# Optimization experiments

Hardware: AMD Instinct MI355X
Metric: run time of the kernel (lower is better)

Reference implementation:

```python
import jax, jax.numpy as jnp
import numpy as np

N = 4096          # vocab / support size (Nini == Nfin)
NBB = 64          # number of topics (columns of b)
NUM_ITER_MAX = 30
STOP_THR = 1e-9


def setup_inputs() -> dict:
    key = jax.random.key(0)
    k1, k2, k3, k4 = jax.random.split(key, 4)
    a = jax.random.uniform(k1, (N, 1), dtype=jnp.float32)
    a = a / jnp.sum(a)                       # source distribution
    b = jax.random.uniform(k2, (N, NBB), dtype=jnp.float32)
    b = b / jnp.sum(b, axis=0, keepdims=True)  # each column a distribution
    lbd = jax.random.uniform(k3, (NBB, 1), dtype=jnp.float32)
    lbd = lbd / jnp.sum(lbd)                 # barycenter weights sum to 1
    M = jax.random.uniform(k4, (N, N), dtype=jnp.float32)  # cost matrix >= 0
    reg = jnp.float32(0.1)
    return {"a": a, "M": M, "b": b, "lbd": lbd, "reg": reg}


def reference(a, M, b, lbd, reg):
    C = jnp.exp(-M / reg)                    # expjit
    lbdT = lbd.T                             # (1, nbb)
    u0 = jnp.ones_like(b)                    # (N, nbb)
    v0 = jnp.ones_like(b)                    # (N, nbb)
    yhat0 = jnp.zeros_like(a)                # (N, 1)

    def cond(state):
        cpt, err, broke, u, v, yhat = state
        return (err > STOP_THR) & (cpt < NUM_ITER_MAX) & (~broke)

    def body(state):
        cpt, err, broke, u, v, yhat = state
        Cu = C @ u                                        # (N, nbb)
        v_new = C.T @ (b / Cu)                            # (N, nbb)
        yhat_new = jnp.prod(v_new ** lbdT, axis=1, keepdims=True)  # (N, 1)
        u_new = yhat_new / v_new                          # (N, nbb)
        bad = (jnp.any(Cu == 0)
               | ~jnp.all(jnp.isfinite(u_new))
               | ~jnp.all(jnp.isfinite(v_new))
               | ~jnp.all(jnp.isfinite(yhat_new)))
        # convergence check every 10 iterations (torch: cpt % 10 == 0)
        lhs = jnp.sum((u_new - u) ** 2) / jnp.sum(u_new ** 2)
        rhs = jnp.sum((v_new - v) ** 2) / jnp.sum(v_new ** 2)
        err_new = jnp.where((cpt % 10 == 0) & ~bad, lhs + rhs, err)
        # on numerical error: revert to previous iterates and break
        u2 = jnp.where(bad, u, u_new)
        v2 = jnp.where(bad, v, v_new)
        yhat2 = jnp.where(bad, yhat, yhat_new)
        cpt2 = cpt + jnp.where(bad, 0, 1)
        return (cpt2, err_new, bad, u2, v2, yhat2)

    state0 = (jnp.int32(0), jnp.float32(1.0), jnp.bool_(False), u0, v0, yhat0)
    *_, yhat = jax.lax.while_loop(cond, body, state0)
    # torch.norm(yhat - a) ** 2 == squared Frobenius norm
    return jnp.sum((yhat - a) ** 2)
```

## Files before the change

### kernel.cpp

```cpp
#include <hip/hip_runtime.h>


typedef __attribute__((ext_vector_type(8))) short bf16x8;
typedef __attribute__((ext_vector_type(4))) float f32x4;

constexpr int NV    = 4096;
constexpr int NBB_  = 64;
constexpr int ITERS = 30;

__device__ __forceinline__ bool finitef(float x) {
  return __builtin_fabsf(x) <= 3.402823466e38f;
}

__device__ __forceinline__ unsigned short f2bf(float x) {
  unsigned int u = __builtin_bit_cast(unsigned int, x);
  return (unsigned short)((u + 0x7fffu + ((u >> 16) & 1u)) >> 16);
}

__global__ void k_setup(float* __restrict__ u, float* __restrict__ v,
                        unsigned short* __restrict__ uT, float* __restrict__ yh,
                        float* __restrict__ S) {
  const int gid = blockIdx.x * 256 + threadIdx.x;
  for (int i = gid; i < NV * NBB_; i += 16384) {
    u[i] = 1.0f; v[i] = 1.0f; uT[i] = 0x3F80;
  }
  for (int i = gid; i < NV; i += 16384) yh[i] = 0.0f;
  if (gid == 0) {
    int* Si = (int*)S;
    S[0]  = 1.0f;
    Si[1] = 0;
    Si[2] = 0;
    Si[3] = 1; Si[4] = 0;
    Si[5] = 0; Si[6] = 0;
    Si[7] = 0; Si[8] = 0;
    for (int q = 16; q < 16 + ITERS; ++q) Si[q] = 0;
  }
}

__global__ void k_cgen(const float* __restrict__ M, const float* __restrict__ regp,
                       unsigned short* __restrict__ Cb,
                       unsigned short* __restrict__ CTb) {
  __shared__ float tile[64][65];
  const int jb = (blockIdx.x & 63) * 64;
  const int ib = (blockIdx.x >> 6) * 64;
  const float ninv = -1.0f / regp[0];
  const int t = threadIdx.x;
#pragma unroll
  for (int s = 0; s < 4; ++s) {
    const int l = s * 256 + t;
    const int r = l >> 4, c4 = l & 15;
    const float4 m4 = *(const float4*)&M[(size_t)(ib + r) * NV + jb + c4 * 4];
    float4 e4;
    e4.x = __expf(m4.x * ninv);
    e4.y = __expf(m4.y * ninv);
    e4.z = __expf(m4.z * ninv);
    e4.w = __expf(m4.w * ninv);
    ushort4 o;
    o.x = f2bf(e4.x); o.y = f2bf(e4.y); o.z = f2bf(e4.z); o.w = f2bf(e4.w);
    *(ushort4*)&Cb[(size_t)(ib + r) * NV + jb + c4 * 4] = o;
    *(float4*)&tile[r][c4 * 4] = e4;
  }
  __syncthreads();
#pragma unroll
  for (int s = 0; s < 4; ++s) {
    const int l = s * 256 + t;
    const int r = l >> 4, c4 = l & 15;
    ushort4 o;
    o.x = f2bf(tile[c4 * 4 + 0][r]);
    o.y = f2bf(tile[c4 * 4 + 1][r]);
    o.z = f2bf(tile[c4 * 4 + 2][r]);
    o.w = f2bf(tile[c4 * 4 + 3][r]);
    *(ushort4*)&CTb[(size_t)(jb + r) * NV + ib + c4 * 4] = o;
  }
}

#define GEMM_CORE(Abase, Bbase, red4)                                          \
  {                                                                            \
    const unsigned short* Ap = (Abase) + (size_t)(R + lr) * NV + w * 512 + lg * 8; \
    const unsigned short* Bp = (Bbase) + (size_t)lr * NV + w * 512 + lg * 8;   \
    f32x4 acc[4] = {};                                                         \
    bf16x8 abuf[3];                                                            \
    bf16x8 bbuf[3][4];                                                         \
    _Pragma("unroll")                                                          \
    for (int p = 0; p < 3; ++p) {                                              \
      abuf[p] = *(const bf16x8*)(Ap + 32 * p);                                 \
      _Pragma("unroll")                                                        \
      for (int ct = 0; ct < 4; ++ct)                                           \
        bbuf[p][ct] = *(const bf16x8*)(Bp + (size_t)ct * 16 * NV + 32 * p);    \
    }                                                                          \
    _Pragma("unroll")                                                          \
    for (int i = 0; i < 16; ++i) {                                             \
      const int sl = i % 3;                                                    \
      _Pragma("unroll")                                                        \
      for (int ct = 0; ct < 4; ++ct)                                           \
        acc[ct] = __builtin_amdgcn_mfma_f32_16x16x32_bf16(abuf[sl],            \
                                                          bbuf[sl][ct],        \
                                                          acc[ct], 0, 0, 0);   \
      if (i + 3 < 16) {                                                        \
        abuf[sl] = *(const bf16x8*)(Ap + 32 * (i + 3));                        \
        _Pragma("unroll")                                                      \
        for (int ct = 0; ct < 4; ++ct)                                         \
          bbuf[sl][ct] =                                                       \
              *(const bf16x8*)(Bp + (size_t)ct * 16 * NV + 32 * (i + 3));      \
      }                                                                        \
    }                                                                          \
    _Pragma("unroll")                                                          \
    for (int ct = 0; ct < 4; ++ct) red4[w][ct][lane] = acc[ct];                \
  }

__global__ __launch_bounds__(512, 2) void k_fwd1(
    const unsigned short* __restrict__ Cb, const unsigned short* __restrict__ uT,
    const float* __restrict__ b, unsigned short* __restrict__ rT,
    int* __restrict__ badflag, const int* __restrict__ act) {
  if (*act == 0) return;
  __shared__ f32x4 red4[8][4][64];
  const int R = blockIdx.x * 16;
  const int t = threadIdx.x, w = t >> 6, lane = t & 63;
  const int lr = lane & 15, lg = lane >> 4;
  GEMM_CORE(Cb, uT, red4)
  __syncthreads();
  if (w < 4) {
    const int ct = w;
    f32x4 cu = red4[0][ct][lane];
#pragma unroll
    for (int j = 1; j < 8; ++j) cu += red4[j][ct][lane];
    bool bad = false;
    float rq[4];
#pragma unroll
    for (int q = 0; q < 4; ++q) {
      const float cuq = cu[q];
      const float bq  = b[(R + lg * 4 + q) * NBB_ + ct * 16 + lr];
      bad |= (cuq == 0.0f);
      rq[q] = bq / cuq;
    }
    ushort4 rr;
    rr.x = f2bf(rq[0]); rr.y = f2bf(rq[1]); rr.z = f2bf(rq[2]); rr.w = f2bf(rq[3]);
    *(ushort4*)&rT[(size_t)(ct * 16 + lr) * NV + R + lg * 4] = rr;
    if (bad) atomicOr(badflag, 1);
  }
}

__global__ __launch_bounds__(512, 2) void k_fwd2(
    const unsigned short* __restrict__ CTb, const unsigned short* __restrict__ rT,
    const float* __restrict__ lbd, float* __restrict__ u, float* __restrict__ v,
    unsigned short* __restrict__ uT, float* __restrict__ yh,
    float* __restrict__ yhn, float* __restrict__ Spart, float* __restrict__ S,
    int it) {
  int* Si = (int*)S;
  const int slot = it & 1;
  if (Si[3 + slot] == 0) {
    if (blockIdx.x == 0 && threadIdx.x == 0) Si[3 + (slot ^ 1)] = 0;
    return;
  }
  __shared__ f32x4 red4[8][4][64];
  __shared__ float yred[4][16];
  __shared__ float yhl[16];
  __shared__ float wred[4][4];
  __shared__ float cred[8][4];
  __shared__ int   flags[2];
  const int R = blockIdx.x * 16;
  const int t = threadIdx.x, w = t >> 6, lane = t & 63;
  const int lr = lane & 15, lg = lane >> 4;
  GEMM_CORE(CTb, rT, red4)
  __syncthreads();
  f32x4 vv = {0.f, 0.f, 0.f, 0.f};
  if (w < 4) {
    vv = red4[0][w][lane];
#pragma unroll
    for (int j = 1; j < 8; ++j) vv += red4[j][w][lane];
    const float lb = lbd[w * 16 + lr];
    float p[4];
#pragma unroll
    for (int q = 0; q < 4; ++q) p[q] = lb * __logf(vv[q]);
#pragma unroll
    for (int o = 1; o < 16; o <<= 1) {
#pragma unroll
      for (int q = 0; q < 4; ++q) p[q] += __shfl_xor(p[q], o);
    }
    if (lr == 0) {
#pragma unroll
      for (int q = 0; q < 4; ++q) yred[w][lg * 4 + q] = p[q];
    }
  }
  __syncthreads();
  if (t < 16) {
    const float s   = yred[0][t] + yred[1][t] + yred[2][t] + yred[3][t];
    const float yhv = __expf(s);
    yhl[t] = yhv;
    yhn[R + t] = yhv;
    if (!finitef(yhv)) atomicOr(&Si[7 + slot], 1);
  }
  __syncthreads();
  if (w < 4) {
    float s0 = 0.f, s1 = 0.f, s2 = 0.f, s3 = 0.f;
    bool bad = false;
    float un4[4];
#pragma unroll
    for (int q = 0; q < 4; ++q) {
      const int   row = lg * 4 + q;
      const float yhv = yhl[row];
      const float un  = yhv / vv[q];
      un4[q] = un;
      const int idx = (R + row) * NBB_ + w * 16 + lr;
      const float uo = u[idx], vo = v[idx];
      u[idx] = un;
      v[idx] = vv[q];
      const float du = un - uo, dv = vv[q] - vo;
      s0 += du * du; s1 += un * un; s2 += dv * dv; s3 += vv[q] * vv[q];
      bad |= !(finitef(un) && finitef(vv[q]));
    }
    ushort4 uu;
    uu.x = f2bf(un4[0]); uu.y = f2bf(un4[1]); uu.z = f2bf(un4[2]); uu.w = f2bf(un4[3]);
    *(ushort4*)&uT[(size_t)(w * 16 + lr) * NV + R + lg * 4] = uu;
    if (bad) atomicOr(&Si[7 + slot], 1);
#pragma unroll
    for (int o = 1; o < 64; o <<= 1) {
      s0 += __shfl_xor(s0, o); s1 += __shfl_xor(s1, o);
      s2 += __shfl_xor(s2, o); s3 += __shfl_xor(s3, o);
    }
    if (lane == 0) {
      wred[w][0] = s0; wred[w][1] = s1; wred[w][2] = s2; wred[w][3] = s3;
    }
  }
  __syncthreads();
  if (t == 0) {
#pragma unroll
    for (int c = 0; c < 4; ++c)
      Spart[blockIdx.x * 4 + c] =
          wred[0][c] + wred[1][c] + wred[2][c] + wred[3][c];
    __threadfence();
    flags[0] = (atomicAdd(&Si[16 + it], 1) == (int)gridDim.x - 1);
  }
  __syncthreads();
  if (!flags[0]) return;
  __threadfence();
  {
    const int c   = t & 3;
    const int idx = t >> 2;
    float s = Spart[idx * 4 + c] + Spart[(idx + 128) * 4 + c];
#pragma unroll
    for (int o = 4; o < 64; o <<= 1) s += __shfl_xor(s, o);
    if (lane < 4) cred[w][lane] = s;
  }
  __syncthreads();
  if (t == 0) {
    float q0 = 0.f, q1 = 0.f, q2 = 0.f, q3 = 0.f;
#pragma unroll
    for (int i = 0; i < 8; ++i) {
      q0 += cred[i][0]; q1 += cred[i][1]; q2 += cred[i][2]; q3 += cred[i][3];
    }
    const bool bad = (Si[5 + slot] | Si[7 + slot]) != 0;
    int com = 0;
    if (!bad) {
      const int cpt = Si[1];
      if (cpt % 10 == 0) S[0] = q0 / q1 + q2 / q3;
      Si[1] = cpt + 1;
      com = 1;
    } else {
      Si[2] = 1;
    }
    const int ns = slot ^ 1;
    Si[3 + ns] = (S[0] > 1e-9f && Si[1] < ITERS && Si[2] == 0) ? 1 : 0;
    Si[5 + ns] = 0;
    Si[7 + ns] = 0;
    flags[1] = com;
  }
  __syncthreads();
  if (flags[1])
    for (int i = t; i < NV; i += 512) yh[i] = yhn[i];
}

__global__ void k_final(const float* __restrict__ yhat, const float* __restrict__ a,
                        float* __restrict__ out) {
  __shared__ float red[4];
  const int t = threadIdx.x;
  float s = 0.0f;
  for (int i = t; i < NV; i += 256) {
    const float d = yhat[i] - a[i];
    s = fmaf(d, d, s);
  }
#pragma unroll
  for (int o = 32; o > 0; o >>= 1) s += __shfl_xor(s, o);
  if ((t & 63) == 0) red[t >> 6] = s;
  __syncthreads();
  if (t == 0) out[0] = red[0] + red[1] + red[2] + red[3];
}

extern "C" void kernel_launch(void* const* d_in, const int* in_sizes, int n_in,
                              void* d_out, int out_size, void* d_ws, size_t ws_size,
                              hipStream_t stream) {
  const float* a   = (const float*)d_in[0];
  const float* M   = (const float*)d_in[1];
  const float* b   = (const float*)d_in[2];
  const float* lbd = (const float*)d_in[3];
  const float* reg = (const float*)d_in[4];
  float* out = (float*)d_out;

  char* wsb = (char*)d_ws;
  size_t off = 0;
  auto alloc = [&](size_t bytes) -> void* {
    void* p = wsb + off;
    off += (bytes + 255) & ~(size_t)255;
    return p;
  };
  unsigned short* Cbf   = (unsigned short*)alloc(2 * (size_t)NV * NV);
  unsigned short* CTbf  = (unsigned short*)alloc(2 * (size_t)NV * NV);
  unsigned short* uT    = (unsigned short*)alloc(2 * (size_t)NV * NBB_);
  unsigned short* rT    = (unsigned short*)alloc(2 * (size_t)NV * NBB_);
  float*          u     = (float*)alloc(sizeof(float) * (size_t)NV * NBB_);
  float*          v     = (float*)alloc(sizeof(float) * (size_t)NV * NBB_);
  float*          yh    = (float*)alloc(sizeof(float) * NV);
  float*          yhn   = (float*)alloc(sizeof(float) * NV);
  float*          S     = (float*)alloc(sizeof(float) * 64);
  float*          Spart = (float*)alloc(sizeof(float) * 256 * 4);
  int* Si = (int*)S;

  k_setup<<<dim3(64), dim3(256), 0, stream>>>(u, v, uT, yh, S);
  k_cgen<<<dim3(4096), dim3(256), 0, stream>>>(M, reg, Cbf, CTbf);

  for (int it = 0; it < ITERS; ++it) {
    const int slot = it & 1;
    const int* act = (const int*)(Si + 3 + slot);
    k_fwd1<<<dim3(256), dim3(512), 0, stream>>>(Cbf, uT, b, rT, Si + 5 + slot, act);
    k_fwd2<<<dim3(256), dim3(512), 0, stream>>>(CTbf, rT, lbd, u, v, uT, yh,
                                                yhn, Spart, S, it);
  }

  k_final<<<dim3(1), dim3(256), 0, stream>>>(yh, a, out);
}
```

Measured before the change: 1.237 ms.

## Fuse iteration loop into one persistent kernel with software grid barriers

Replaces the 60 per-iteration kernel launches plus the final reduction kernel with a single persistent kernel of 256 blocks. The blocks synchronise through a two-level atomic grid barrier, and every block computes the convergence and break state redundantly instead of relying on host-side flags. This targets launch overhead and inter-kernel gaps. It also deepens the load prefetch pipeline in the GEMM core from 3 to 5 stages. The barrier assumes all 256 blocks are co-resident; otherwise it can deadlock. Spin-wait and atomic traffic add some cost per phase.

```diff
diff --git a/kernel.cpp b/kernel.cpp
--- a/kernel.cpp
+++ b/kernel.cpp
@@ -17,24 +17,31 @@
   return (unsigned short)((u + 0x7fffu + ((u >> 16) & 1u)) >> 16);
 }
 
+__device__ __forceinline__ void gbar(int* __restrict__ bar1,
+                                     int* __restrict__ bar2, int jb) {
+  __syncthreads();
+  if (threadIdx.x == 0) {
+    __threadfence();
+    const int g = blockIdx.x & 7;
+    const int n = atomicAdd(&bar1[g * 32], 1);
+    if (n == 32 * jb - 1) atomicAdd(bar2, 1);
+    while (__hip_atomic_load(bar2, __ATOMIC_RELAXED, __HIP_MEMORY_SCOPE_AGENT) <
+           8 * jb)
+      __builtin_amdgcn_s_sleep(2);
+    __threadfence();
+  }
+  __syncthreads();
+}
+
 __global__ void k_setup(float* __restrict__ u, float* __restrict__ v,
                         unsigned short* __restrict__ uT, float* __restrict__ yh,
-                        float* __restrict__ S) {
+                        int* __restrict__ Sctl) {
   const int gid = blockIdx.x * 256 + threadIdx.x;
   for (int i = gid; i < NV * NBB_; i += 16384) {
     u[i] = 1.0f; v[i] = 1.0f; uT[i] = 0x3F80;
   }
   for (int i = gid; i < NV; i += 16384) yh[i] = 0.0f;
-  if (gid == 0) {
-    int* Si = (int*)S;
-    S[0]  = 1.0f;
-    Si[1] = 0;
-    Si[2] = 0;
-    Si[3] = 1; Si[4] = 0;
-    Si[5] = 0; Si[6] = 0;
-    Si[7] = 0; Si[8] = 0;
-    for (int q = 16; q < 16 + ITERS; ++q) Si[q] = 0;
-  }
+  if (gid < 512) Sctl[gid] = 0;
 }
 
 __global__ void k_cgen(const float* __restrict__ M, const float* __restrict__ regp,
@@ -74,15 +81,15 @@
   }
 }
 
-#define GEMM_CORE(Abase, Bbase, red4)                                          \
+#define GEMM_CORE(Abase, Bbase)                                                \
   {                                                                            \
     const unsigned short* Ap = (Abase) + (size_t)(R + lr) * NV + w * 512 + lg * 8; \
     const unsigned short* Bp = (Bbase) + (size_t)lr * NV + w * 512 + lg * 8;   \
     f32x4 acc[4] = {};                                                         \
-    bf16x8 abuf[3];                                                            \
-    bf16x8 bbuf[3][4];                                                         \
+    bf16x8 abuf[5];                                                            \
+    bf16x8 bbuf[5][4];                                                         \
     _Pragma("unroll")                                                          \
-    for (int p = 0; p < 3; ++p) {                                              \
+    for (int p = 0; p < 5; ++p) {                                              \
       abuf[p] = *(const bf16x8*)(Ap + 32 * p);                                 \
       _Pragma("unroll")                                                        \
       for (int ct = 0; ct < 4; ++ct)                                           \
@@ -90,200 +97,194 @@
     }                                                                          \
     _Pragma("unroll")                                                          \
     for (int i = 0; i < 16; ++i) {                                             \
-      const int sl = i % 3;                                                    \
+      const int sl = i % 5;                                                    \
       _Pragma("unroll")                                                        \
       for (int ct = 0; ct < 4; ++ct)                                           \
         acc[ct] = __builtin_amdgcn_mfma_f32_16x16x32_bf16(abuf[sl],            \
                                                           bbuf[sl][ct],        \
                                                           acc[ct], 0, 0, 0);   \
-      if (i + 3 < 16) {                                                        \
-        abuf[sl] = *(const bf16x8*)(Ap + 32 * (i + 3));                        \
+      if (i + 5 < 16) {                                                        \
+        abuf[sl] = *(const bf16x8*)(Ap + 32 * (i + 5));                        \
         _Pragma("unroll")                                                      \
         for (int ct = 0; ct < 4; ++ct)                                         \
           bbuf[sl][ct] =                                                       \
-              *(const bf16x8*)(Bp + (size_t)ct * 16 * NV + 32 * (i + 3));      \
+              *(const bf16x8*)(Bp + (size_t)ct * 16 * NV + 32 * (i + 5));      \
       }                                                                        \
     }                                                                          \
     _Pragma("unroll")                                                          \
     for (int ct = 0; ct < 4; ++ct) red4[w][ct][lane] = acc[ct];                \
   }
 
-__global__ __launch_bounds__(512, 2) void k_fwd1(
-    const unsigned short* __restrict__ Cb, const unsigned short* __restrict__ uT,
-    const float* __restrict__ b, unsigned short* __restrict__ rT,
-    int* __restrict__ badflag, const int* __restrict__ act) {
-  if (*act == 0) return;
-  __shared__ f32x4 red4[8][4][64];
-  const int R = blockIdx.x * 16;
-  const int t = threadIdx.x, w = t >> 6, lane = t & 63;
-  const int lr = lane & 15, lg = lane >> 4;
-  GEMM_CORE(Cb, uT, red4)
-  __syncthreads();
-  if (w < 4) {
-    const int ct = w;
-    f32x4 cu = red4[0][ct][lane];
-#pragma unroll
-    for (int j = 1; j < 8; ++j) cu += red4[j][ct][lane];
-    bool bad = false;
-    float rq[4];
-#pragma unroll
-    for (int q = 0; q < 4; ++q) {
-      const float cuq = cu[q];
-      const float bq  = b[(R + lg * 4 + q) * NBB_ + ct * 16 + lr];
-      bad |= (cuq == 0.0f);
-      rq[q] = bq / cuq;
-    }
-    ushort4 rr;
-    rr.x = f2bf(rq[0]); rr.y = f2bf(rq[1]); rr.z = f2bf(rq[2]); rr.w = f2bf(rq[3]);
-    *(ushort4*)&rT[(size_t)(ct * 16 + lr) * NV + R + lg * 4] = rr;
-    if (bad) atomicOr(badflag, 1);
-  }
-}
-
-__global__ __launch_bounds__(512, 2) void k_fwd2(
-    const unsigned short* __restrict__ CTb, const unsigned short* __restrict__ rT,
-    const float* __restrict__ lbd, float* __restrict__ u, float* __restrict__ v,
-    unsigned short* __restrict__ uT, float* __restrict__ yh,
-    float* __restrict__ yhn, float* __restrict__ Spart, float* __restrict__ S,
-    int it) {
-  int* Si = (int*)S;
-  const int slot = it & 1;
-  if (Si[3 + slot] == 0) {
-    if (blockIdx.x == 0 && threadIdx.x == 0) Si[3 + (slot ^ 1)] = 0;
-    return;
-  }
+__global__ __launch_bounds__(512, 2) void k_persist(
+    const unsigned short* __restrict__ Cb, const unsigned short* __restrict__ CTb,
+    const float* __restrict__ b, const float* __restrict__ lbd,
+    const float* __restrict__ a, float* __restrict__ u, float* __restrict__ v,
+    unsigned short* __restrict__ uT, unsigned short* __restrict__ rT,
+    float* __restrict__ yh, float* __restrict__ Spart, int* __restrict__ bar1,
+    int* __restrict__ bar2, int* __restrict__ badf, float* __restrict__ out) {
   __shared__ f32x4 red4[8][4][64];
   __shared__ float yred[4][16];
   __shared__ float yhl[16];
   __shared__ float wred[4][4];
-  __shared__ float cred[8][4];
-  __shared__ int   flags[2];
+  __shared__ float cred[4][4];
+  __shared__ float fred[8];
+  __shared__ float serr;
+  __shared__ int   sbad;
   const int R = blockIdx.x * 16;
   const int t = threadIdx.x, w = t >> 6, lane = t & 63;
   const int lr = lane & 15, lg = lane >> 4;
-  GEMM_CORE(CTb, rT, red4)
-  __syncthreads();
-  f32x4 vv = {0.f, 0.f, 0.f, 0.f};
-  if (w < 4) {
-    vv = red4[0][w][lane];
-#pragma unroll
-    for (int j = 1; j < 8; ++j) vv += red4[j][w][lane];
-    const float lb = lbd[w * 16 + lr];
-    float p[4];
-#pragma unroll
-    for (int q = 0; q < 4; ++q) p[q] = lb * __logf(vv[q]);
-#pragma unroll
-    for (int o = 1; o < 16; o <<= 1) {
-#pragma unroll
-      for (int q = 0; q < 4; ++q) p[q] += __shfl_xor(p[q], o);
-    }
-    if (lr == 0) {
-#pragma unroll
-      for (int q = 0; q < 4; ++q) yred[w][lg * 4 + q] = p[q];
-    }
-  }
-  __syncthreads();
-  if (t < 16) {
-    const float s   = yred[0][t] + yred[1][t] + yred[2][t] + yred[3][t];
-    const float yhv = __expf(s);
-    yhl[t] = yhv;
-    yhn[R + t] = yhv;
-    if (!finitef(yhv)) atomicOr(&Si[7 + slot], 1);
-  }
-  __syncthreads();
-  if (w < 4) {
-    float s0 = 0.f, s1 = 0.f, s2 = 0.f, s3 = 0.f;
-    bool bad = false;
-    float un4[4];
-#pragma unroll
-    for (int q = 0; q < 4; ++q) {
-      const int   row = lg * 4 + q;
-      const float yhv = yhl[row];
-      const float un  = yhv / vv[q];
-      un4[q] = un;
-      const int idx = (R + row) * NBB_ + w * 16 + lr;
-      const float uo = u[idx], vo = v[idx];
-      u[idx] = un;
-      v[idx] = vv[q];
-      const float du = un - uo, dv = vv[q] - vo;
-      s0 += du * du; s1 += un * un; s2 += dv * dv; s3 += vv[q] * vv[q];
-      bad |= !(finitef(un) && finitef(vv[q]));
-    }
-    ushort4 uu;
-    uu.x = f2bf(un4[0]); uu.y = f2bf(un4[1]); uu.z = f2bf(un4[2]); uu.w = f2bf(un4[3]);
-    *(ushort4*)&uT[(size_t)(w * 16 + lr) * NV + R + lg * 4] = uu;
-    if (bad) atomicOr(&Si[7 + slot], 1);
-#pragma unroll
-    for (int o = 1; o < 64; o <<= 1) {
-      s0 += __shfl_xor(s0, o); s1 += __shfl_xor(s1, o);
-      s2 += __shfl_xor(s2, o); s3 += __shfl_xor(s3, o);
-    }
-    if (lane == 0) {
-      wred[w][0] = s0; wred[w][1] = s1; wred[w][2] = s2; wred[w][3] = s3;
-    }
-  }
-  __syncthreads();
-  if (t == 0) {
-#pragma unroll
-    for (int c = 0; c < 4; ++c)
-      Spart[blockIdx.x * 4 + c] =
-          wred[0][c] + wred[1][c] + wred[2][c] + wred[3][c];
-    __threadfence();
-    flags[0] = (atomicAdd(&Si[16 + it], 1) == (int)gridDim.x - 1);
-  }
-  __syncthreads();
-  if (!flags[0]) return;
-  __threadfence();
-  {
-    const int c   = t & 3;
-    const int idx = t >> 2;
-    float s = Spart[idx * 4 + c] + Spart[(idx + 128) * 4 + c];
-#pragma unroll
-    for (int o = 4; o < 64; o <<= 1) s += __shfl_xor(s, o);
-    if (lane < 4) cred[w][lane] = s;
-  }
-  __syncthreads();
-  if (t == 0) {
-    float q0 = 0.f, q1 = 0.f, q2 = 0.f, q3 = 0.f;
-#pragma unroll
-    for (int i = 0; i < 8; ++i) {
-      q0 += cred[i][0]; q1 += cred[i][1]; q2 += cred[i][2]; q3 += cred[i][3];
-    }
-    const bool bad = (Si[5 + slot] | Si[7 + slot]) != 0;
-    int com = 0;
-    if (!bad) {
-      const int cpt = Si[1];
-      if (cpt % 10 == 0) S[0] = q0 / q1 + q2 / q3;
-      Si[1] = cpt + 1;
-      com = 1;
+  float err = 1.0f;
+  int cpt = 0, nb = 0;
+  bool broke = false;
+
+  for (int it = 0; it < ITERS; ++it) {
+    GEMM_CORE(Cb, uT)
+    __syncthreads();
+    if (w < 4) {
+      f32x4 cu = red4[0][w][lane];
+#pragma unroll
+      for (int j = 1; j < 8; ++j) cu += red4[j][w][lane];
+      bool badl = false;
+      float rq[4];
+#pragma unroll
+      for (int q = 0; q < 4; ++q) {
+        const float cuq = cu[q];
+        const float bq  = b[(R + lg * 4 + q) * NBB_ + w * 16 + lr];
+        badl |= (cuq == 0.0f);
+        rq[q] = bq / cuq;
+      }
+      ushort4 rr;
+      rr.x = f2bf(rq[0]); rr.y = f2bf(rq[1]);
+      rr.z = f2bf(rq[2]); rr.w = f2bf(rq[3]);
+      *(ushort4*)&rT[(size_t)(w * 16 + lr) * NV + R + lg * 4] = rr;
+      if (badl) atomicOr(&badf[it], 1);
+    }
+    ++nb; gbar(bar1, bar2, nb);
+
+    GEMM_CORE(CTb, rT)
+    __syncthreads();
+    f32x4 vv = {0.f, 0.f, 0.f, 0.f};
+    if (w < 4) {
+      vv = red4[0][w][lane];
+#pragma unroll
+      for (int j = 1; j < 8; ++j) vv += red4[j][w][lane];
+      const float lb = lbd[w * 16 + lr];
+      float p[4];
+#pragma unroll
+      for (int q = 0; q < 4; ++q) p[q] = lb * __logf(vv[q]);
+#pragma unroll
+      for (int o = 1; o < 16; o <<= 1) {
+#pragma unroll
+        for (int q = 0; q < 4; ++q) p[q] += __shfl_xor(p[q], o);
+      }
+      if (lr == 0) {
+#pragma unroll
+        for (int q = 0; q < 4; ++q) yred[w][lg * 4 + q] = p[q];
+      }
+    }
+    __syncthreads();
+    if (t < 16) {
+      const float s   = yred[0][t] + yred[1][t] + yred[2][t] + yred[3][t];
+      const float yhv = __expf(s);
+      yhl[t] = yhv;
+      if (!finitef(yhv)) atomicOr(&badf[it], 1);
+    }
+    __syncthreads();
+    if (w < 4) {
+      float s0 = 0.f, s1 = 0.f, s2 = 0.f, s3 = 0.f;
+      bool badl = false;
+      float un4[4];
+#pragma unroll
+      for (int q = 0; q < 4; ++q) {
+        const int   row = lg * 4 + q;
+        const float yhv = yhl[row];
+        const float un  = yhv / vv[q];
+        un4[q] = un;
+        const int idx = (R + row) * NBB_ + w * 16 + lr;
+        const float uo = u[idx], vo = v[idx];
+        u[idx] = un;
+        v[idx] = vv[q];
+        const float du = un - uo, dv = vv[q] - vo;
+        s0 += du * du; s1 += un * un; s2 += dv * dv; s3 += vv[q] * vv[q];
+        badl |= !(finitef(un) && finitef(vv[q]));
+      }
+      ushort4 uu;
+      uu.x = f2bf(un4[0]); uu.y = f2bf(un4[1]);
+      uu.z = f2bf(un4[2]); uu.w = f2bf(un4[3]);
+      *(ushort4*)&uT[(size_t)(w * 16 + lr) * NV + R + lg * 4] = uu;
+      if (badl) atomicOr(&badf[it], 1);
+#pragma unroll
+      for (int o = 1; o < 64; o <<= 1) {
+        s0 += __shfl_xor(s0, o); s1 += __shfl_xor(s1, o);
+        s2 += __shfl_xor(s2, o); s3 += __shfl_xor(s3, o);
+      }
+      if (lane == 0) {
+        wred[w][0] = s0; wred[w][1] = s1; wred[w][2] = s2; wred[w][3] = s3;
+      }
+    }
+    __syncthreads();
+    if (t == 0) {
+#pragma unroll
+      for (int c = 0; c < 4; ++c)
+        Spart[blockIdx.x * 4 + c] =
+            wred[0][c] + wred[1][c] + wred[2][c] + wred[3][c];
+    }
+    ++nb; gbar(bar1, bar2, nb);
+
+    if (t == 0)
+      sbad = __hip_atomic_load(&badf[it], __ATOMIC_RELAXED,
+                               __HIP_MEMORY_SCOPE_AGENT);
+    __syncthreads();
+    if (sbad == 0) {
+      if (cpt % 10 == 0) {
+        float4 sp = make_float4(0.f, 0.f, 0.f, 0.f);
+        if (t < 256) sp = ((const float4*)Spart)[t];
+        float s0 = sp.x, s1 = sp.y, s2 = sp.z, s3 = sp.w;
+#pragma unroll
+        for (int o = 1; o < 64; o <<= 1) {
+          s0 += __shfl_xor(s0, o); s1 += __shfl_xor(s1, o);
+          s2 += __shfl_xor(s2, o); s3 += __shfl_xor(s3, o);
+        }
+        if (lane == 0 && w < 4) {
+          cred[w][0] = s0; cred[w][1] = s1; cred[w][2] = s2; cred[w][3] = s3;
+        }
+        __syncthreads();
+        if (t == 0) {
+          const float q0 = cred[0][0] + cred[1][0] + cred[2][0] + cred[3][0];
+          const float q1 = cred[0][1] + cred[1][1] + cred[2][1] + cred[3][1];
+          const float q2 = cred[0][2] + cred[1][2] + cred[2][2] + cred[3][2];
+          const float q3 = cred[0][3] + cred[1][3] + cred[2][3] + cred[3][3];
+          serr = q0 / q1 + q2 / q3;
+        }
+        __syncthreads();
+        err = serr;
+      }
+      ++cpt;
+      if (t < 16) yh[R + t] = yhl[t];
     } else {
-      Si[2] = 1;
-    }
-    const int ns = slot ^ 1;
-    Si[3 + ns] = (S[0] > 1e-9f && Si[1] < ITERS && Si[2] == 0) ? 1 : 0;
-    Si[5 + ns] = 0;
-    Si[7 + ns] = 0;
-    flags[1] = com;
-  }
-  __syncthreads();
-  if (flags[1])
-    for (int i = t; i < NV; i += 512) yh[i] = yhn[i];
-}
-
-__global__ void k_final(const float* __restrict__ yhat, const float* __restrict__ a,
-                        float* __restrict__ out) {
-  __shared__ float red[4];
-  const int t = threadIdx.x;
-  float s = 0.0f;
-  for (int i = t; i < NV; i += 256) {
-    const float d = yhat[i] - a[i];
-    s = fmaf(d, d, s);
-  }
-#pragma unroll
-  for (int o = 32; o > 0; o >>= 1) s += __shfl_xor(s, o);
-  if ((t & 63) == 0) red[t >> 6] = s;
-  __syncthreads();
-  if (t == 0) out[0] = red[0] + red[1] + red[2] + red[3];
+      broke = true;
+    }
+    if (broke || !(err > 1e-9f) || cpt >= ITERS) break;
+  }
+
+  ++nb; gbar(bar1, bar2, nb);
+  if (blockIdx.x == 0) {
+    float s = 0.0f;
+    for (int i = t; i < NV; i += 512) {
+      const float d = yh[i] - a[i];
+      s = fmaf(d, d, s);
+    }
+#pragma unroll
+    for (int o = 1; o < 64; o <<= 1) s += __shfl_xor(s, o);
+    if (lane == 0) fred[w] = s;
+    __syncthreads();
+    if (t == 0) {
+      float q = 0.0f;
+#pragma unroll
+      for (int i = 0; i < 8; ++i) q += fred[i];
+      out[0] = q;
+    }
+  }
 }
 
 extern "C" void kernel_launch(void* const* d_in, const int* in_sizes, int n_in,
@@ -310,21 +311,15 @@
   float*          u     = (float*)alloc(sizeof(float) * (size_t)NV * NBB_);
   float*          v     = (float*)alloc(sizeof(float) * (size_t)NV * NBB_);
   float*          yh    = (float*)alloc(sizeof(float) * NV);
-  float*          yhn   = (float*)alloc(sizeof(float) * NV);
-  float*          S     = (float*)alloc(sizeof(float) * 64);
   float*          Spart = (float*)alloc(sizeof(float) * 256 * 4);
-  int* Si = (int*)S;
-
-  k_setup<<<dim3(64), dim3(256), 0, stream>>>(u, v, uT, yh, S);
+  int*            Sctl  = (int*)alloc(sizeof(int) * 512);
+  int* bar1 = Sctl;
+  int* bar2 = Sctl + 256;
+  int* badf = Sctl + 288;
+
+  k_setup<<<dim3(64), dim3(256), 0, stream>>>(u, v, uT, yh, Sctl);
   k_cgen<<<dim3(4096), dim3(256), 0, stream>>>(M, reg, Cbf, CTbf);
-
-  for (int it = 0; it < ITERS; ++it) {
-    const int slot = it & 1;
-    const int* act = (const int*)(Si + 3 + slot);
-    k_fwd1<<<dim3(256), dim3(512), 0, stream>>>(Cbf, uT, b, rT, Si + 5 + slot, act);
-    k_fwd2<<<dim3(256), dim3(512), 0, stream>>>(CTbf, rT, lbd, u, v, uT, yh,
-                                                yhn, Spart, S, it);
-  }
-
-  k_final<<<dim3(1), dim3(256), 0, stream>>>(yh, a, out);
-}
+  k_persist<<<dim3(256), dim3(512), 0, stream>>>(Cbf, CTbf, b, lbd, a, u, v,
+                                                 uT, rT, yh, Spart, bar1, bar2,
+                                                 badf, out);
+}
```

New measurement: 1.476 ms. +19.3%, slower.
